# Optimization experiments

Hardware: AMD Instinct MI355X
Metric: run time of the kernel (lower is better)

## Reference

```python
import jax, jax.numpy as jnp
import numpy as np

# static sinkhorn parameters (match SamplesLoss init kwargs)
P = 2
BLUR = 0.05
SCALING = 0.5
DIAMETER = 2.0  # points on the unit sphere => diameter <= 2

# geomloss epsilon_schedule: [diameter^p] + exp(arange(p*log(d), p*log(blur), p*log(scaling))) + [blur^p]
EPS_LIST = (
    [DIAMETER ** P]
    + [float(np.exp(e)) for e in np.arange(P * np.log(DIAMETER), P * np.log(BLUR), P * np.log(SCALING))]
    + [BLUR ** P]
)


def cost(m, n):
    # spherical (geodesic) distance / 2 between unit vectors: acos(<m,n>)/2
    t = jnp.clip(jnp.einsum('bnd,bmd->bnm', m, n), -1.0 + 1e-6, 1.0 - 1e-6)
    return jnp.arccos(t) * 0.5  # (B,N,M)


def softmin(eps, C, wlog):
    # -eps * logsumexp(wlog[B,1,M] - C/eps, axis=2) -> (B,N)
    return -eps * jax.nn.logsumexp(wlog[:, None, :] - C / eps, axis=2)


def log_weights(a):
    return jnp.where(a > 0, jnp.log(jnp.maximum(a, 1e-30)), -1e5)


def setup_inputs() -> dict:
    key = jax.random.key(0)
    kx, ky = jax.random.split(key)
    B, N, M, D = 8, 2048, 2048, 3
    x = jax.random.normal(kx, (B, N, D), dtype=jnp.float32)
    y = jax.random.normal(ky, (B, M, D), dtype=jnp.float32)
    # project onto the unit sphere (spherical cost assumes unit vectors)
    x = x / jnp.linalg.norm(x, axis=-1, keepdims=True)
    y = y / jnp.linalg.norm(y, axis=-1, keepdims=True)
    alpha = jnp.ones((B, N), dtype=jnp.float32) / N
    beta = jnp.ones((B, M), dtype=jnp.float32) / M
    return {"alpha": alpha, "x": x, "beta": beta, "y": y}


def reference(alpha, x, beta, y):
    sg = jax.lax.stop_gradient
    # second argument of each cost is detached, as in the torch code
    C_xx = cost(x, sg(x))
    C_yy = cost(y, sg(y))
    C_xy = cost(x, sg(y))
    C_yx = cost(y, sg(x))
    al = log_weights(alpha)
    bl = log_weights(beta)

    # ---- sinkhorn loop (torch.no_grad section) ----
    Cxx_, Cyy_, Cxy_, Cyx_, al_, bl_ = map(sg, (C_xx, C_yy, C_xy, C_yx, al, bl))
    eps = EPS_LIST[0]
    a_x = softmin(eps, Cxx_, al_)   # OT(a,a) potential on x
    b_y = softmin(eps, Cyy_, bl_)   # OT(b,b) potential on y
    a_y = softmin(eps, Cyx_, al_)   # OT(a,b) potential on y
    b_x = softmin(eps, Cxy_, bl_)   # OT(a,b) potential on x
    for eps in EPS_LIST:  # annealed, symmetrized sinkhorn updates
        at_x = softmin(eps, Cxx_, al_ + a_x / eps)
        bt_y = softmin(eps, Cyy_, bl_ + b_y / eps)
        at_y = softmin(eps, Cyx_, al_ + b_x / eps)
        bt_x = softmin(eps, Cxy_, bl_ + a_y / eps)
        a_x, b_y = 0.5 * (a_x + at_x), 0.5 * (b_y + bt_y)
        a_y, b_x = 0.5 * (a_y + at_y), 0.5 * (b_x + bt_x)

    # ---- last extrapolation, differentiable (eps = blur^p) ----
    eps = EPS_LIST[-1]
    a_x = softmin(eps, C_xx, sg(al + a_x / eps))
    b_y = softmin(eps, C_yy, sg(bl + b_y / eps))
    a_y = softmin(eps, C_yx, sg(al + b_x / eps))
    b_x = softmin(eps, C_xy, sg(bl + a_y / eps))

    # balanced (reach=None), debiased sinkhorn cost -> (B,)
    return jnp.sum(alpha * (b_x - a_x), axis=-1) + jnp.sum(beta * (a_y - b_y), axis=-1)
```

## Files before the change

### kernel.cpp

```cpp
#include <hip/hip_runtime.h>
#include <math.h>

#define BB 8
#define NN 2048
#define L2E 1.4426950408889634f
#define LN2 0.6931471805599453f
#define PI_F 3.14159265358979f
#define CLIP 0.999999f
#define THSC 20860.0f
#define THSCI (1.0f / 20860.0f)

constexpr int TB   = 128;
constexpr int T16  = NN / TB;
constexpr int NXX  = T16 * (T16 + 1) / 2;
constexpr int NT   = 2 * NXX + T16 * T16;
constexpr int SARR = BB * NN;

__device__ __forceinline__ void decode_tile(int bx, int& kind, int& I, int& J) {
    if (bx < NXX) kind = 0;
    else if (bx < 2 * NXX) { kind = 1; bx -= NXX; }
    else { kind = 2; bx -= 2 * NXX; }
    if (kind < 2) {
        int idx = bx; I = 0;
        for (;;) { int len = T16 - I; if (idx < len) { J = I + idx; break; } idx -= len; I++; }
    } else { I = bx >> 4; J = bx & 15; }
}

__device__ __forceinline__ float acos_raw(float d) {
    const float u = fabsf(d);
    float pl = fmaf(u, -0.0187293f, 0.0742610f);
    pl = fmaf(u, pl, -0.2121144f); pl = fmaf(u, pl, 1.5707288f);
    const float rt = __builtin_amdgcn_sqrtf(1.f - u) * pl;
    return (d >= 0.f) ? rt : (PI_F - rt);
}

__device__ __forceinline__ size_t th_off(int g, int wv, int lane) {
    return (size_t)(((g * 4 + wv) * 64 + lane) * 8);
}

__global__ __launch_bounds__(256)
void pack_kernel(const float* __restrict__ alpha, const float* __restrict__ beta,
                 float* __restrict__ gxw, float* __restrict__ gyw,
                 float* __restrict__ Wall, float* __restrict__ Gall)
{
    const int tid = threadIdx.x;
    const int gid = blockIdx.x * 256 + tid;
    const int o = gid >> 14, i = gid & (SARR - 1);
    const float* w = (o == 0 || o == 3) ? alpha : beta;
    const float v = w[i];
    const float g = ((v > 0.f) ? logf(fmaxf(v, 1e-30f)) : -1e5f) * L2E;
    if (o == 0) gxw[i] = g;
    if (o == 1) gyw[i] = g;
    __shared__ float red[256];
    red[tid] = g;
    __syncthreads();
    const int base = tid & 128, loc = tid & 127;
    for (int st = 64; st; st >>= 1) {
        if (loc < st) red[base + loc] = fmaxf(red[base + loc], red[base + loc + st]);
        __syncthreads();
    }
    const float G = red[base];
    Wall[gid] = __builtin_amdgcn_exp2f(g - G);
    if (loc == 0) Gall[gid >> 7] = G;
}

__global__ __launch_bounds__(256)
void maxes_kernel(const float* __restrict__ x, const float* __restrict__ y,
                  float* __restrict__ Rxx, float* __restrict__ Ryy,
                  float* __restrict__ Rxy, float* __restrict__ Cxy,
                  unsigned short* __restrict__ Theta, int writeTheta)
{
    __shared__ float4 p1s[TB], p2s[TB];
    __shared__ float colred[4][TB];
    int kind, I, J; decode_tile(blockIdx.x, kind, I, J);
    const int b = blockIdx.y, t = threadIdx.x;
    const float* P1 = (kind == 1) ? y : x;
    const float* P2 = (kind == 0) ? x : y;
    if (t < TB) {
        size_t gi = (size_t)b * NN + (size_t)I * TB + t;
        p1s[t] = make_float4(P1[gi * 3], P1[gi * 3 + 1], P1[gi * 3 + 2], 0.f);
    } else {
        int u = t - TB; size_t gi = (size_t)b * NN + (size_t)J * TB + u;
        p2s[u] = make_float4(P2[gi * 3], P2[gi * 3 + 1], P2[gi * 3 + 2], 0.f);
    }
    __syncthreads();
    const int lane = t & 63, wv = t >> 6, colg = lane & 7, rowg = lane >> 3;
    const int r0 = wv * 32 + rowg * 4;
    unsigned short* Tb = Theta + ((size_t)(b * NT + blockIdx.x) << 14);

    float4 pr[4];
#pragma unroll
    for (int rr = 0; rr < 4; rr++) pr[rr] = p1s[r0 + rr];
    float rmx[4] = {-2.f, -2.f, -2.f, -2.f};
    float cmx[16];
#pragma unroll
    for (int j = 0; j < 16; j++) cmx[j] = -2.f;

#pragma unroll
    for (int g = 0; g < 8; g++) {
        uint4 outv;
#pragma unroll
        for (int e = 0; e < 2; e++) {
            const int j = g * 2 + e;
            const float4 q = p2s[colg + 8 * j];
            unsigned int lo = 0, hi = 0;
#pragma unroll
            for (int rr = 0; rr < 4; rr++) {
                const float d = fmaf(pr[rr].x, q.x, fmaf(pr[rr].y, q.y, pr[rr].z * q.z));
                rmx[rr] = fmaxf(rmx[rr], d);
                cmx[j] = fmaxf(cmx[j], d);
                if (writeTheta) {
                    const float dc = fminf(fmaxf(d, -CLIP), CLIP);
                    const unsigned int qv = __float2uint_rn(acos_raw(dc) * THSC);
                    if (rr == 0) lo = qv;
                    else if (rr == 1) lo |= qv << 16;
                    else if (rr == 2) hi = qv;
                    else hi |= qv << 16;
                }
            }
            if (e == 0) { outv.x = lo; outv.y = hi; }
            else        { outv.z = lo; outv.w = hi; }
        }
        if (writeTheta)
            *(uint4*)(Tb + th_off(g, wv, lane)) = outv;
    }

#pragma unroll
    for (int rr = 0; rr < 4; rr++) {
        float v = rmx[rr];
        v = fmaxf(v, __shfl_xor(v, 1)); v = fmaxf(v, __shfl_xor(v, 2));
        v = fmaxf(v, __shfl_xor(v, 4));
        rmx[rr] = v;
    }
    if (colg == 0) {
        float* R = (kind == 0) ? Rxx : (kind == 1) ? Ryy : Rxy;
        const size_t base = ((size_t)b * T16 + J) * NN + (size_t)I * TB + r0;
#pragma unroll
        for (int rr = 0; rr < 4; rr++)
            R[base + rr] = acos_raw(fminf(fmaxf(rmx[rr], -CLIP), CLIP));
    }
#pragma unroll
    for (int j = 0; j < 16; j++) {
        float v = cmx[j];
        v = fmaxf(v, __shfl_xor(v, 8)); v = fmaxf(v, __shfl_xor(v, 16));
        v = fmaxf(v, __shfl_xor(v, 32));
        cmx[j] = v;
    }
    if (rowg == 0) {
#pragma unroll
        for (int j = 0; j < 16; j++) colred[wv][colg + 8 * j] = cmx[j];
    }
    __syncthreads();
    if (t < TB) {
        const float v = fmaxf(fmaxf(colred[0][t], colred[1][t]),
                              fmaxf(colred[2][t], colred[3][t]));
        const float th = acos_raw(fminf(fmaxf(v, -CLIP), CLIP));
        if (kind == 2) {
            Cxy[((size_t)b * T16 + I) * NN + (size_t)J * TB + t] = th;
        } else if (I != J) {
            float* R = (kind == 0) ? Rxx : Ryy;
            R[((size_t)b * T16 + I) * NN + (size_t)J * TB + t] = th;
        }
    }
}

struct TileArgsT {
    const unsigned short* Theta;
    const float* Wall; const float* Gall;
    const float* Rxx; const float* Ryy; const float* Rxy; const float* Cxy;
    float2* pAX; float2* pBY; float2* pAY; float2* pBX;
};

__global__ __launch_bounds__(256)
void tile_theta_kernel(TileArgsT A, float ieh, float Kq)
{
    __shared__ float2 s1[TB], s2[TB];
    __shared__ float colpart[4][TB];
    int kind, I, J; decode_tile(blockIdx.x, kind, I, J);
    const int b = blockIdx.y, t = threadIdx.x;
    const int o1 = (kind == 0) ? 0 : (kind == 1) ? 1 : 3;
    const int o2 = (kind == 0) ? 0 : (kind == 1) ? 1 : 2;
    float2* rowOut = (kind == 0) ? A.pAX : (kind == 1) ? A.pBY : A.pBX;
    float2* colOut = (kind == 0) ? A.pAX : (kind == 1) ? A.pBY : A.pAY;
    const bool diag = (kind < 2) && (I == J);
    const float* W1 = A.Wall + (size_t)o1 * SARR;
    const float* W2 = A.Wall + (size_t)o2 * SARR;
    const float* Rrow = (kind == 0) ? A.Rxx : (kind == 1) ? A.Ryy : A.Rxy;
    const float* Csrc = (kind == 0) ? A.Rxx : (kind == 1) ? A.Ryy : A.Cxy;

    if (t < TB) {
        size_t gi = (size_t)b * NN + (size_t)I * TB + t;
        s1[t] = make_float2(Rrow[((size_t)b * T16 + J) * NN + (size_t)I * TB + t] * ieh, W1[gi]);
    } else {
        int u = t - TB; size_t gi = (size_t)b * NN + (size_t)J * TB + u;
        s2[u] = make_float2(Csrc[((size_t)b * T16 + I) * NN + (size_t)J * TB + u] * ieh, W2[gi]);
    }
    const float G1 = A.Gall[o1 * 128 + b * T16 + I];
    const float G2 = A.Gall[o2 * 128 + b * T16 + J];
    __syncthreads();

    const int lane = t & 63, wv = t >> 6, colg = lane & 7, rowg = lane >> 3;
    const int r0 = wv * 32 + rowg * 4;
    const unsigned short* Tb = A.Theta + ((size_t)(b * NT + blockIdx.x) << 14);

    float srr[4], w1r[4];
#pragma unroll
    for (int rr = 0; rr < 4; rr++) { const float2 v = s1[r0 + rr]; srr[rr] = v.x; w1r[rr] = v.y; }
    float racc[4] = {0.f, 0.f, 0.f, 0.f};
    float cacc[16];
#pragma unroll
    for (int j = 0; j < 16; j++) cacc[j] = 0.f;

#pragma unroll
    for (int g = 0; g < 8; g++) {
        const uint4 tq = *(const uint4*)(Tb + th_off(g, wv, lane));
#pragma unroll
        for (int e = 0; e < 2; e++) {
            const int j = g * 2 + e;
            const unsigned int lo = e ? tq.z : tq.x;
            const unsigned int hi = e ? tq.w : tq.y;
            const float2 sv = s2[colg + 8 * j];
            const float thv[4] = {
                (float)(lo & 0xffffu), (float)(lo >> 16),
                (float)(hi & 0xffffu), (float)(hi >> 16)
            };
#pragma unroll
            for (int rr = 0; rr < 4; rr++) {
                const float er = __builtin_amdgcn_exp2f(fmaf(thv[rr], -Kq, srr[rr]));
                const float ec = __builtin_amdgcn_exp2f(fmaf(thv[rr], -Kq, sv.x));
                racc[rr] = fmaf(sv.y, er, racc[rr]);
                cacc[j]  = fmaf(w1r[rr], ec, cacc[j]);
            }
        }
    }

#pragma unroll
    for (int j = 0; j < 16; j++) {
        float v = cacc[j];
        v += __shfl_xor(v, 8); v += __shfl_xor(v, 16); v += __shfl_xor(v, 32);
        cacc[j] = v;
    }
    if (rowg == 0) {
#pragma unroll
        for (int j = 0; j < 16; j++) colpart[wv][colg + 8 * j] = cacc[j];
    }
#pragma unroll
    for (int rr = 0; rr < 4; rr++) {
        float v = racc[rr];
        v += __shfl_xor(v, 1); v += __shfl_xor(v, 2); v += __shfl_xor(v, 4);
        racc[rr] = v;
    }
    if (colg == 0) {
        const size_t gr = (size_t)J * SARR + (size_t)b * NN + (size_t)I * TB + r0;
#pragma unroll
        for (int rr = 0; rr < 4; rr++)
            rowOut[gr + rr] = make_float2(G2 - srr[rr], racc[rr]);
    }
    __syncthreads();
    if (!diag && t < TB) {
        const float v = colpart[0][t] + colpart[1][t] + colpart[2][t] + colpart[3][t];
        const size_t gc = (size_t)I * SARR + (size_t)b * NN + (size_t)J * TB + t;
        colOut[gc] = make_float2(G1 - s2[t].x, v);
    }
}

struct TileArgs {
    const float* x; const float* y;
    const float* Wall; const float* Gall;
    const float* Rxx; const float* Ryy; const float* Rxy; const float* Cxy;
    float2* pAX; float2* pBY; float2* pAY; float2* pBX;
};

__global__ __launch_bounds__(256)
void tile_kernel(TileArgs A, float ieh, float pi_ieh)
{
    __shared__ float4 p1s[TB], p2s[TB];
    __shared__ float srs[TB], scs[TB];
    __shared__ float colpart[4][TB];
    int kind, I, J; decode_tile(blockIdx.x, kind, I, J);
    const int b = blockIdx.y, t = threadIdx.x;
    const float* P1 = (kind == 1) ? A.y : A.x;
    const float* P2 = (kind == 0) ? A.x : A.y;
    const int o1 = (kind == 0) ? 0 : (kind == 1) ? 1 : 3;
    const int o2 = (kind == 0) ? 0 : (kind == 1) ? 1 : 2;
    float2* rowOut = (kind == 0) ? A.pAX : (kind == 1) ? A.pBY : A.pBX;
    float2* colOut = (kind == 0) ? A.pAX : (kind == 1) ? A.pBY : A.pAY;
    const bool diag = (kind < 2) && (I == J);
    const float* W1 = A.Wall + (size_t)o1 * SARR;
    const float* W2 = A.Wall + (size_t)o2 * SARR;
    const float* Rrow = (kind == 0) ? A.Rxx : (kind == 1) ? A.Ryy : A.Rxy;
    const float* Csrc = (kind == 0) ? A.Rxx : (kind == 1) ? A.Ryy : A.Cxy;

    const float K0 = 1.5707288f * ieh, K1 = -0.2121144f * ieh;
    const float K2 = 0.0742610f * ieh, K3 = -0.0187293f * ieh;

    if (t < TB) {
        size_t gi = (size_t)b * NN + (size_t)I * TB + t;
        p1s[t] = make_float4(P1[gi * 3], P1[gi * 3 + 1], P1[gi * 3 + 2], W1[gi]);
        srs[t] = Rrow[((size_t)b * T16 + J) * NN + (size_t)I * TB + t] * ieh;
    } else {
        int u = t - TB; size_t gi = (size_t)b * NN + (size_t)J * TB + u;
        p2s[u] = make_float4(P2[gi * 3], P2[gi * 3 + 1], P2[gi * 3 + 2], W2[gi]);
        scs[u] = Csrc[((size_t)b * T16 + I) * NN + (size_t)J * TB + u] * ieh;
    }
    const float G1 = A.Gall[o1 * 128 + b * T16 + I];
    const float G2 = A.Gall[o2 * 128 + b * T16 + J];
    __syncthreads();

    const int lane = t & 63, wv = t >> 6, colg = lane & 7, rowg = lane >> 3;
    const int r0 = wv * 32 + rowg * 4;
    float4 pr[4]; float srr[4];
#pragma unroll
    for (int rr = 0; rr < 4; rr++) { pr[rr] = p1s[r0 + rr]; srr[rr] = srs[r0 + rr]; }
    float racc[4] = {0.f, 0.f, 0.f, 0.f};
    float cacc[16];
#pragma unroll
    for (int j = 0; j < 16; j++) cacc[j] = 0.f;

#pragma unroll
    for (int j = 0; j < 16; j++) {
        const float4 q = p2s[colg + 8 * j];
        const float sc = scs[colg + 8 * j];
#pragma unroll
        for (int rr = 0; rr < 4; rr++) {
            const float4 p = pr[rr];
            float d = fmaf(p.x, q.x, fmaf(p.y, q.y, p.z * q.z));
            d = fminf(fmaxf(d, -CLIP), CLIP);
            const float u = fabsf(d);
            float pl = fmaf(u, K3, K2); pl = fmaf(u, pl, K1); pl = fmaf(u, pl, K0);
            const float rt = __builtin_amdgcn_sqrtf(1.f - u) * pl;
            const float ach = (d >= 0.f) ? rt : (pi_ieh - rt);
            racc[rr] = fmaf(q.w, __builtin_amdgcn_exp2f(srr[rr] - ach), racc[rr]);
            cacc[j]  = fmaf(p.w, __builtin_amdgcn_exp2f(sc - ach), cacc[j]);
        }
    }

#pragma unroll
    for (int j = 0; j < 16; j++) {
        float v = cacc[j];
        v += __shfl_xor(v, 8); v += __shfl_xor(v, 16); v += __shfl_xor(v, 32);
        cacc[j] = v;
    }
    if (rowg == 0) {
#pragma unroll
        for (int j = 0; j < 16; j++) colpart[wv][colg + 8 * j] = cacc[j];
    }
#pragma unroll
    for (int rr = 0; rr < 4; rr++) {
        float v = racc[rr];
        v += __shfl_xor(v, 1); v += __shfl_xor(v, 2); v += __shfl_xor(v, 4);
        racc[rr] = v;
    }
    if (colg == 0) {
        const size_t gr = (size_t)J * SARR + (size_t)b * NN + (size_t)I * TB + r0;
#pragma unroll
        for (int rr = 0; rr < 4; rr++)
            rowOut[gr + rr] = make_float2(G2 - srr[rr], racc[rr]);
    }
    __syncthreads();
    if (!diag && t < TB) {
        const float v = colpart[0][t] + colpart[1][t] + colpart[2][t] + colpart[3][t];
        const size_t gc = (size_t)I * SARR + (size_t)b * NN + (size_t)J * TB + t;
        colOut[gc] = make_float2(G1 - scs[t], v);
    }
}

__global__ __launch_bounds__(256)
void combine_kernel(const float2* __restrict__ pAX, const float2* __restrict__ pBY,
                    const float2* __restrict__ pAY, const float2* __restrict__ pBX,
                    float* __restrict__ ax, float* __restrict__ by,
                    float* __restrict__ ay, float* __restrict__ bx,
                    const float* __restrict__ gxw, const float* __restrict__ gyw,
                    float* __restrict__ Wall, float* __restrict__ Gall,
                    float eps_ln2, float nieL2E, int do_avg)
{
    const int tid = threadIdx.x;
    const int gid = blockIdx.x * 256 + tid;
    const int o = gid >> 14, i = gid & (SARR - 1);
    const float2* P = (o == 0) ? pAX : (o == 1) ? pBY : (o == 2) ? pAY : pBX;
    float* pot = (o == 0) ? ax : (o == 1) ? by : (o == 2) ? ay : bx;
    float2 pr[T16];
#pragma unroll
    for (int u = 0; u < T16; u++) pr[u] = P[(size_t)u * SARR + i];
    float M = -3.0e38f;
#pragma unroll
    for (int u = 0; u < T16; u++) M = fmaxf(M, (pr[u].y > 0.f) ? pr[u].x : -3.0e38f);
    float S = 0.f;
#pragma unroll
    for (int u = 0; u < T16; u++)
        S += pr[u].y * __builtin_amdgcn_exp2f(fminf(pr[u].x - M, 0.f));
    S = fmaxf(S, 1e-38f);
    float r = -eps_ln2 * (M + __builtin_amdgcn_logf(S));
    if (do_avg) r = 0.5f * (r + pot[i]);
    pot[i] = r;
    const float g = ((o == 0 || o == 3) ? gxw[i] : gyw[i]) + r * nieL2E;
    __shared__ float red[256];
    red[tid] = g;
    __syncthreads();
    const int base = tid & 128, loc = tid & 127;
    for (int st = 64; st; st >>= 1) {
        if (loc < st) red[base + loc] = fmaxf(red[base + loc], red[base + loc + st]);
        __syncthreads();
    }
    const float G = red[base];
    Wall[gid] = __builtin_amdgcn_exp2f(g - G);
    if (loc == 0) Gall[gid >> 7] = G;
}

__global__ __launch_bounds__(256)
void reduce_kernel(const float* __restrict__ alpha, const float* __restrict__ beta,
                   const float* __restrict__ a_x, const float* __restrict__ b_x,
                   const float* __restrict__ a_y, const float* __restrict__ b_y,
                   float* __restrict__ out)
{
    const int b = blockIdx.x, tid = threadIdx.x;
    float acc = 0.f;
    for (int n = tid; n < NN; n += 256) {
        const size_t i = (size_t)b * NN + n;
        acc += alpha[i] * (b_x[i] - a_x[i]);
        acc += beta[i] * (a_y[i] - b_y[i]);
    }
    __shared__ float red[256];
    red[tid] = acc;
    __syncthreads();
    for (int st = 128; st > 0; st >>= 1) {
        if (tid < st) red[tid] += red[tid + st];
        __syncthreads();
    }
    if (tid == 0) out[b] = red[0];
}

extern "C" void kernel_launch(void* const* d_in, const int* in_sizes, int n_in,
                              void* d_out, int out_size, void* d_ws, size_t ws_size,
                              hipStream_t stream)
{
    const float* alpha = (const float*)d_in[0];
    const float* x     = (const float*)d_in[1];
    const float* beta  = (const float*)d_in[2];
    const float* y     = (const float*)d_in[3];
    float* out = (float*)d_out;
    float* ws  = (float*)d_ws;

    const size_t S = SARR;
    float* gxw  = ws;
    float* gyw  = ws + S;
    float* ax   = ws + 2 * S;
    float* by   = ws + 3 * S;
    float* ay   = ws + 4 * S;
    float* bx   = ws + 5 * S;
    float* Wall = ws + 6 * S;
    float* Gall = ws + 10 * S;
    float* Rxx  = ws + 10 * S + 512;
    float* Ryy  = Rxx + 16 * S;
    float* Rxy  = Ryy + 16 * S;
    float* Cxy  = Rxy + 16 * S;
    float* pb   = Cxy + 16 * S;
    const size_t PSZ = (size_t)SARR * T16;
    float2* pAX = (float2*)pb;
    float2* pBY = pAX + PSZ;
    float2* pAY = pBY + PSZ;
    float2* pBX = pAY + PSZ;

    float* thetaF = pb + (size_t)8 * PSZ;
    unsigned short* Theta = (unsigned short*)thetaF;
    const size_t used_bytes  = (size_t)((char*)thetaF - (char*)ws);
    const size_t theta_bytes = (size_t)BB * NT * 16384 * sizeof(unsigned short);
    const int useTheta = (ws_size >= used_bytes + theta_bytes) ? 1 : 0;

    const float EPS[8] = {4.0f, 4.0f, 1.0f, 0.25f, 0.0625f, 0.015625f, 0.00390625f, 0.0025f};

    pack_kernel<<<(4 * SARR) / 256, 256, 0, stream>>>(alpha, beta, gxw, gyw, Wall, Gall);
    maxes_kernel<<<dim3(NT, BB), 256, 0, stream>>>(x, y, Rxx, Ryy, Rxy, Cxy, Theta, useTheta);

    TileArgsT TT;
    TT.Theta = Theta; TT.Wall = Wall; TT.Gall = Gall;
    TT.Rxx = Rxx; TT.Ryy = Ryy; TT.Rxy = Rxy; TT.Cxy = Cxy;
    TT.pAX = pAX; TT.pBY = pBY; TT.pAY = pAY; TT.pBX = pBX;

    TileArgs TA;
    TA.x = x; TA.y = y; TA.Wall = Wall; TA.Gall = Gall;
    TA.Rxx = Rxx; TA.Ryy = Ryy; TA.Rxy = Rxy; TA.Cxy = Cxy;
    TA.pAX = pAX; TA.pBY = pBY; TA.pAY = pAY; TA.pBX = pBX;

    auto step = [&](float e, float next_e, int avg) {
        const float ieh = 0.5f * (1.f / e) * L2E;
        if (useTheta)
            tile_theta_kernel<<<dim3(NT, BB), 256, 0, stream>>>(TT, ieh, ieh * THSCI);
        else
            tile_kernel<<<dim3(NT, BB), 256, 0, stream>>>(TA, ieh, PI_F * ieh);
        combine_kernel<<<(4 * SARR) / 256, 256, 0, stream>>>(
            pAX, pBY, pAY, pBX, ax, by, ay, bx, gxw, gyw, Wall, Gall,
            e * LN2, (1.f / next_e) * L2E, avg);
    };

    step(EPS[0], EPS[0], 0);
    for (int k = 0; k < 8; k++) step(EPS[k], (k < 7) ? EPS[k + 1] : EPS[7], 1);
    step(EPS[7], EPS[7], 0);

    reduce_kernel<<<BB, 256, 0, stream>>>(alpha, beta, ax, bx, ay, by, out);
}
```

Before: 430.5 us.

## Fuse first softmin into maxes kernel and halve exp count in theta tiles

```diff
diff --git a/kernel.cpp b/kernel.cpp
--- a/kernel.cpp
+++ b/kernel.cpp
@@ -68,21 +68,35 @@
 void maxes_kernel(const float* __restrict__ x, const float* __restrict__ y,
                   float* __restrict__ Rxx, float* __restrict__ Ryy,
                   float* __restrict__ Rxy, float* __restrict__ Cxy,
-                  unsigned short* __restrict__ Theta, int writeTheta)
+                  unsigned short* __restrict__ Theta,
+                  const float* __restrict__ Wall, const float* __restrict__ Gall,
+                  float2* pAX, float2* pBY, float2* pAY, float2* pBX,
+                  float negK, int writeTheta)
 {
     __shared__ float4 p1s[TB], p2s[TB];
     __shared__ float colred[4][TB];
+    __shared__ float colpart[4][TB];
     int kind, I, J; decode_tile(blockIdx.x, kind, I, J);
     const int b = blockIdx.y, t = threadIdx.x;
     const float* P1 = (kind == 1) ? y : x;
     const float* P2 = (kind == 0) ? x : y;
+    const int o1 = (kind == 0) ? 0 : (kind == 1) ? 1 : 3;
+    const int o2 = (kind == 0) ? 0 : (kind == 1) ? 1 : 2;
+    float2* rowOut = (kind == 0) ? pAX : (kind == 1) ? pBY : pBX;
+    float2* colOut = (kind == 0) ? pAX : (kind == 1) ? pBY : pAY;
+    const bool diag = (kind < 2) && (I == J);
+    const float* W1 = Wall + (size_t)o1 * SARR;
+    const float* W2 = Wall + (size_t)o2 * SARR;
+
     if (t < TB) {
         size_t gi = (size_t)b * NN + (size_t)I * TB + t;
-        p1s[t] = make_float4(P1[gi * 3], P1[gi * 3 + 1], P1[gi * 3 + 2], 0.f);
+        p1s[t] = make_float4(P1[gi * 3], P1[gi * 3 + 1], P1[gi * 3 + 2], W1[gi]);
     } else {
         int u = t - TB; size_t gi = (size_t)b * NN + (size_t)J * TB + u;
-        p2s[u] = make_float4(P2[gi * 3], P2[gi * 3 + 1], P2[gi * 3 + 2], 0.f);
-    }
+        p2s[u] = make_float4(P2[gi * 3], P2[gi * 3 + 1], P2[gi * 3 + 2], W2[gi]);
+    }
+    const float G1 = Gall[o1 * 128 + b * T16 + I];
+    const float G2 = Gall[o2 * 128 + b * T16 + J];
     __syncthreads();
     const int lane = t & 63, wv = t >> 6, colg = lane & 7, rowg = lane >> 3;
     const int r0 = wv * 32 + rowg * 4;
@@ -95,6 +109,10 @@
     float cmx[16];
 #pragma unroll
     for (int j = 0; j < 16; j++) cmx[j] = -2.f;
+    float racc[4] = {0.f, 0.f, 0.f, 0.f};
+    float cacc[16];
+#pragma unroll
+    for (int j = 0; j < 16; j++) cacc[j] = 0.f;
 
 #pragma unroll
     for (int g = 0; g < 8; g++) {
@@ -111,11 +129,15 @@
                 cmx[j] = fmaxf(cmx[j], d);
                 if (writeTheta) {
                     const float dc = fminf(fmaxf(d, -CLIP), CLIP);
-                    const unsigned int qv = __float2uint_rn(acos_raw(dc) * THSC);
+                    const float th = acos_raw(dc);
+                    const unsigned int qv = __float2uint_rn(th * THSC);
                     if (rr == 0) lo = qv;
                     else if (rr == 1) lo |= qv << 16;
                     else if (rr == 2) hi = qv;
                     else hi |= qv << 16;
+                    const float em = __builtin_amdgcn_exp2f(th * negK);
+                    racc[rr] = fmaf(q.w, em, racc[rr]);
+                    cacc[j]  = fmaf(pr[rr].w, em, cacc[j]);
                 }
             }
             if (e == 0) { outv.x = lo; outv.y = hi; }
@@ -150,6 +172,32 @@
 #pragma unroll
         for (int j = 0; j < 16; j++) colred[wv][colg + 8 * j] = cmx[j];
     }
+
+    if (writeTheta) {
+#pragma unroll
+        for (int j = 0; j < 16; j++) {
+            float v = cacc[j];
+            v += __shfl_xor(v, 8); v += __shfl_xor(v, 16); v += __shfl_xor(v, 32);
+            cacc[j] = v;
+        }
+        if (rowg == 0) {
+#pragma unroll
+            for (int j = 0; j < 16; j++) colpart[wv][colg + 8 * j] = cacc[j];
+        }
+#pragma unroll
+        for (int rr = 0; rr < 4; rr++) {
+            float v = racc[rr];
+            v += __shfl_xor(v, 1); v += __shfl_xor(v, 2); v += __shfl_xor(v, 4);
+            racc[rr] = v;
+        }
+        if (colg == 0) {
+            const size_t gr = (size_t)J * SARR + (size_t)b * NN + (size_t)I * TB + r0;
+#pragma unroll
+            for (int rr = 0; rr < 4; rr++)
+                rowOut[gr + rr] = make_float2(G2, racc[rr]);
+        }
+    }
+
     __syncthreads();
     if (t < TB) {
         const float v = fmaxf(fmaxf(colred[0][t], colred[1][t]),
@@ -161,6 +209,11 @@
             float* R = (kind == 0) ? Rxx : Ryy;
             R[((size_t)b * T16 + I) * NN + (size_t)J * TB + t] = th;
         }
+        if (writeTheta && !diag) {
+            const float pv = colpart[0][t] + colpart[1][t] + colpart[2][t] + colpart[3][t];
+            const size_t gc = (size_t)I * SARR + (size_t)b * NN + (size_t)J * TB + t;
+            colOut[gc] = make_float2(G1, pv);
+        }
     }
 }
 
@@ -174,7 +227,10 @@
 __global__ __launch_bounds__(256)
 void tile_theta_kernel(TileArgsT A, float ieh, float Kq)
 {
-    __shared__ float2 s1[TB], s2[TB];
+    __shared__ float2 s1[TB];
+    __shared__ float2 wq2[TB];
+    __shared__ float  scF[TB];
+    __shared__ float  wps[TB];
     __shared__ float colpart[4][TB];
     int kind, I, J; decode_tile(blockIdx.x, kind, I, J);
     const int b = blockIdx.y, t = threadIdx.x;
@@ -188,24 +244,41 @@
     const float* Rrow = (kind == 0) ? A.Rxx : (kind == 1) ? A.Ryy : A.Rxy;
     const float* Csrc = (kind == 0) ? A.Rxx : (kind == 1) ? A.Ryy : A.Cxy;
 
+    float myW = 0.f, mySc = 0.f;
     if (t < TB) {
         size_t gi = (size_t)b * NN + (size_t)I * TB + t;
-        s1[t] = make_float2(Rrow[((size_t)b * T16 + J) * NN + (size_t)I * TB + t] * ieh, W1[gi]);
+        myW = W1[gi];
+        s1[t] = make_float2(Rrow[((size_t)b * T16 + J) * NN + (size_t)I * TB + t] * ieh, myW);
     } else {
         int u = t - TB; size_t gi = (size_t)b * NN + (size_t)J * TB + u;
-        s2[u] = make_float2(Csrc[((size_t)b * T16 + I) * NN + (size_t)J * TB + u] * ieh, W2[gi]);
+        myW = W2[gi];
+        mySc = Csrc[((size_t)b * T16 + I) * NN + (size_t)J * TB + u] * ieh;
+        scF[u] = mySc;
     }
     const float G1 = A.Gall[o1 * 128 + b * T16 + I];
     const float G2 = A.Gall[o2 * 128 + b * T16 + J];
+    __syncthreads();
+    const float Z2 = 0.5f * s1[0].x;
+    if (t < TB) {
+        wps[t] = myW * __builtin_amdgcn_exp2f(Z2 - 0.5f * s1[t].x);
+    } else {
+        int u = t - TB;
+        wq2[u] = make_float2(0.5f * mySc,
+                             myW * __builtin_amdgcn_exp2f(Z2 - 0.5f * mySc));
+    }
     __syncthreads();
 
     const int lane = t & 63, wv = t >> 6, colg = lane & 7, rowg = lane >> 3;
     const int r0 = wv * 32 + rowg * 4;
     const unsigned short* Tb = A.Theta + ((size_t)(b * NT + blockIdx.x) << 14);
 
-    float srr[4], w1r[4];
-#pragma unroll
-    for (int rr = 0; rr < 4; rr++) { const float2 v = s1[r0 + rr]; srr[rr] = v.x; w1r[rr] = v.y; }
+    float srrF[4], srr2[4], wpr[4];
+#pragma unroll
+    for (int rr = 0; rr < 4; rr++) {
+        srrF[rr] = s1[r0 + rr].x;
+        srr2[rr] = 0.5f * srrF[rr];
+        wpr[rr]  = wps[r0 + rr];
+    }
     float racc[4] = {0.f, 0.f, 0.f, 0.f};
     float cacc[16];
 #pragma unroll
@@ -219,17 +292,19 @@
             const int j = g * 2 + e;
             const unsigned int lo = e ? tq.z : tq.x;
             const unsigned int hi = e ? tq.w : tq.y;
-            const float2 sv = s2[colg + 8 * j];
+            const float2 q2 = wq2[colg + 8 * j];
             const float thv[4] = {
                 (float)(lo & 0xffffu), (float)(lo >> 16),
                 (float)(hi & 0xffffu), (float)(hi >> 16)
             };
+            float bs[4];
+#pragma unroll
+            for (int rr = 0; rr < 4; rr++) bs[rr] = srr2[rr] + q2.x;
 #pragma unroll
             for (int rr = 0; rr < 4; rr++) {
-                const float er = __builtin_amdgcn_exp2f(fmaf(thv[rr], -Kq, srr[rr]));
-                const float ec = __builtin_amdgcn_exp2f(fmaf(thv[rr], -Kq, sv.x));
-                racc[rr] = fmaf(sv.y, er, racc[rr]);
-                cacc[j]  = fmaf(w1r[rr], ec, cacc[j]);
+                const float em = __builtin_amdgcn_exp2f(fmaf(thv[rr], -Kq, bs[rr]));
+                racc[rr] = fmaf(q2.y, em, racc[rr]);
+                cacc[j]  = fmaf(wpr[rr], em, cacc[j]);
             }
         }
     }
@@ -242,7 +317,10 @@
     }
     if (rowg == 0) {
 #pragma unroll
-        for (int j = 0; j < 16; j++) colpart[wv][colg + 8 * j] = cacc[j];
+        for (int j = 0; j < 16; j++) {
+            const int c = colg + 8 * j;
+            colpart[wv][c] = cacc[j] * __builtin_amdgcn_exp2f(wq2[c].x - Z2);
+        }
     }
 #pragma unroll
     for (int rr = 0; rr < 4; rr++) {
@@ -254,13 +332,14 @@
         const size_t gr = (size_t)J * SARR + (size_t)b * NN + (size_t)I * TB + r0;
 #pragma unroll
         for (int rr = 0; rr < 4; rr++)
-            rowOut[gr + rr] = make_float2(G2 - srr[rr], racc[rr]);
+            rowOut[gr + rr] = make_float2(G2 - srrF[rr],
+                racc[rr] * __builtin_amdgcn_exp2f(srr2[rr] - Z2));
     }
     __syncthreads();
     if (!diag && t < TB) {
         const float v = colpart[0][t] + colpart[1][t] + colpart[2][t] + colpart[3][t];
         const size_t gc = (size_t)I * SARR + (size_t)b * NN + (size_t)J * TB + t;
-        colOut[gc] = make_float2(G1 - s2[t].x, v);
+        colOut[gc] = make_float2(G1 - scF[t], v);
     }
 }
 
@@ -470,7 +549,10 @@
     const float EPS[8] = {4.0f, 4.0f, 1.0f, 0.25f, 0.0625f, 0.015625f, 0.00390625f, 0.0025f};
 
     pack_kernel<<<(4 * SARR) / 256, 256, 0, stream>>>(alpha, beta, gxw, gyw, Wall, Gall);
-    maxes_kernel<<<dim3(NT, BB), 256, 0, stream>>>(x, y, Rxx, Ryy, Rxy, Cxy, Theta, useTheta);
+    const float negK = -0.5f * (1.f / EPS[0]) * L2E;
+    maxes_kernel<<<dim3(NT, BB), 256, 0, stream>>>(x, y, Rxx, Ryy, Rxy, Cxy, Theta,
+                                                   Wall, Gall, pAX, pBY, pAY, pBX,
+                                                   negK, useTheta);
 
     TileArgsT TT;
     TT.Theta = Theta; TT.Wall = Wall; TT.Gall = Gall;
@@ -482,20 +564,22 @@
     TA.Rxx = Rxx; TA.Ryy = Ryy; TA.Rxy = Rxy; TA.Cxy = Cxy;
     TA.pAX = pAX; TA.pBY = pBY; TA.pAY = pAY; TA.pBX = pBX;
 
-    auto step = [&](float e, float next_e, int avg) {
+    auto step = [&](float e, float next_e, int avg, int run_tile) {
         const float ieh = 0.5f * (1.f / e) * L2E;
-        if (useTheta)
-            tile_theta_kernel<<<dim3(NT, BB), 256, 0, stream>>>(TT, ieh, ieh * THSCI);
-        else
-            tile_kernel<<<dim3(NT, BB), 256, 0, stream>>>(TA, ieh, PI_F * ieh);
+        if (run_tile) {
+            if (useTheta)
+                tile_theta_kernel<<<dim3(NT, BB), 256, 0, stream>>>(TT, ieh, ieh * THSCI);
+            else
+                tile_kernel<<<dim3(NT, BB), 256, 0, stream>>>(TA, ieh, PI_F * ieh);
+        }
         combine_kernel<<<(4 * SARR) / 256, 256, 0, stream>>>(
             pAX, pBY, pAY, pBX, ax, by, ay, bx, gxw, gyw, Wall, Gall,
             e * LN2, (1.f / next_e) * L2E, avg);
     };
 
-    step(EPS[0], EPS[0], 0);
-    for (int k = 0; k < 8; k++) step(EPS[k], (k < 7) ? EPS[k + 1] : EPS[7], 1);
-    step(EPS[7], EPS[7], 0);
+    step(EPS[0], EPS[0], 0, useTheta ? 0 : 1);
+    for (int k = 0; k < 8; k++) step(EPS[k], (k < 7) ? EPS[k + 1] : EPS[7], 1, 1);
+    step(EPS[7], EPS[7], 0, 1);
 
     reduce_kernel<<<BB, 256, 0, stream>>>(alpha, beta, ax, bx, ay, by, out);
 }
```

Measured after the change: 451.8 us. +5.0%, slower.
